# Kernel tuning notes

Hardware: AMD Instinct MI355X
Metric: run time of the kernel (lower is better)

The kernel has to match this reference:

```python
import jax, jax.numpy as jnp
import numpy as np

B, MAX_LEN, H, D = 4, 4096, 32, 128
Q_LEN = 1


def quantize_i8(x):
    # Symmetric per-(b,s,h) int8 quantization along the head dim (Array8Bit-style).
    scale = jnp.max(jnp.abs(x), axis=-1, keepdims=True) / 127.0
    scale = jnp.maximum(scale, 1e-8)
    q = jnp.clip(jnp.round(x / scale), -128, 127).astype(jnp.int8)
    return q, scale


def setup_inputs() -> dict:
    key = jax.random.key(0)
    k0, k1, k2, k3 = jax.random.split(key, 4)
    return {
        "cached_key": jax.random.normal(k0, (B, MAX_LEN, H, D), dtype=jnp.float32),
        "cached_value": jax.random.normal(k1, (B, MAX_LEN, H, D), dtype=jnp.float32),
        "key": jax.random.normal(k2, (B, Q_LEN, H, D), dtype=jnp.float32),
        "value": jax.random.normal(k3, (B, Q_LEN, H, D), dtype=jnp.float32),
        "attention_mask": jnp.ones((B, 1, Q_LEN, MAX_LEN), dtype=jnp.bool_),
        "cache_index": 2048,
    }


def reference(cached_key, cached_value, key, value, attention_mask, cache_index):
    # --- FlaxAttentionModule._concatenate_to_cache (non-sharded decode path) ---
    max_length = cached_key.shape[1]
    cur_index = jnp.asarray(cache_index, dtype=jnp.int32)
    num_updated = key.shape[1]  # query_states.shape[1]

    # KV-cache write: dynamic_update_slice at (0, cur_index, 0, 0)
    key_out = jax.lax.dynamic_update_slice(cached_key, key, (0, cur_index, 0, 0))
    value_out = jax.lax.dynamic_update_slice(cached_value, value, (0, cur_index, 0, 0))

    # pad_mask: positions < cur_index + num_updated are valid
    pad_mask = jnp.broadcast_to(
        jnp.arange(max_length) < cur_index + num_updated,
        (cached_key.shape[0], 1, num_updated, max_length),
    )
    # combine_masks == logical AND of boolean masks
    attn_mask_out = jnp.logical_and(pad_mask, attention_mask)

    # Inline int8 quantization of the updated cache (quantize_kv_cache path)
    key_q, key_scale = quantize_i8(key_out)
    value_q, value_scale = quantize_i8(value_out)

    return key_out, value_out, attn_mask_out, key_q, key_scale, value_q, value_scale
```

## Files before the change

kernel.cpp:

```cpp
#include <hip/hip_runtime.h>

constexpr long long N_ELEM  = 4LL * 4096 * 32 * 128;
constexpr long long N_ROWS  = 4LL * 4096 * 32;
constexpr long long MASK_N  = 4LL * 4096;
constexpr long long SCALE_N = N_ROWS;


typedef float vf4 __attribute__((ext_vector_type(4)));

__global__ __launch_bounds__(256) void kv_update_quant_kernel(
    const float* __restrict__ cached_key,
    const float* __restrict__ cached_value,
    const float* __restrict__ key_new,
    const float* __restrict__ value_new,
    const int*   __restrict__ cache_index,
    float* __restrict__ out)
{
    const int cur  = cache_index[0];
    const int hw   = threadIdx.x >> 5;
    const int lane = threadIdx.x & 31;

    const long long row0 = (((long long)blockIdx.x * 8 + hw) << 2);
    const bool isv = row0 >= N_ROWS;
    const long long r0 = isv ? row0 - N_ROWS : row0;

    const int h0 = (int)(r0 & 31);
    const int s  = (int)((r0 >> 5) & 4095);
    const long long b = r0 >> 17;

    const float* src;
    if (s == cur) {
        src = (isv ? value_new : key_new) + (((b << 5) + (long long)h0) << 7);
    } else {
        src = (isv ? cached_value : cached_key) + (r0 << 7);
    }
    src += (lane << 2);

    vf4 v[4];
#pragma unroll
    for (int j = 0; j < 4; ++j)
        v[j] = __builtin_nontemporal_load(reinterpret_cast<const vf4*>(src + (j << 7)));

    float sc[4];
#pragma unroll
    for (int j = 0; j < 4; ++j) {
        float m = fmaxf(fmaxf(fabsf(v[j].x), fabsf(v[j].y)),
                        fmaxf(fabsf(v[j].z), fabsf(v[j].w)));
#pragma unroll
        for (int off = 16; off >= 1; off >>= 1)
            m = fmaxf(m, __shfl_xor(m, off));
        sc[j] = fmaxf(m / 127.0f, 1e-8f);
    }

    float* out_p = out + (isv ? N_ELEM : 0) + (r0 << 7) + (lane << 2);
    float* q_p   = out + 2 * N_ELEM + MASK_N + (isv ? (N_ELEM + SCALE_N) : 0)
                   + (r0 << 7) + (lane << 2);

#pragma unroll
    for (int j = 0; j < 4; ++j) {
        __builtin_nontemporal_store(v[j], reinterpret_cast<vf4*>(out_p + (j << 7)));
        vf4 q;
        q.x = fminf(fmaxf(rintf(v[j].x / sc[j]), -128.0f), 127.0f);
        q.y = fminf(fmaxf(rintf(v[j].y / sc[j]), -128.0f), 127.0f);
        q.z = fminf(fmaxf(rintf(v[j].z / sc[j]), -128.0f), 127.0f);
        q.w = fminf(fmaxf(rintf(v[j].w / sc[j]), -128.0f), 127.0f);
        __builtin_nontemporal_store(q, reinterpret_cast<vf4*>(q_p + (j << 7)));
    }

    if (lane == 0) {
        float* s_p = out + 3 * N_ELEM + MASK_N + (isv ? (N_ELEM + SCALE_N) : 0) + r0;
        vf4 sv;
        sv.x = sc[0]; sv.y = sc[1]; sv.z = sc[2]; sv.w = sc[3];
        __builtin_nontemporal_store(sv, reinterpret_cast<vf4*>(s_p));
    }
}

__global__ __launch_bounds__(256) void mask_kernel(
    const int* __restrict__ attention_mask,
    const int* __restrict__ cache_index,
    float* __restrict__ out_mask)
{
    const int i = blockIdx.x * 256 + threadIdx.x;
    if (i < (int)MASK_N) {
        const int pos = i & 4095;
        const bool pad = pos < (cache_index[0] + 1);
        const bool am  = attention_mask[i] != 0;
        out_mask[i] = (pad && am) ? 1.0f : 0.0f;
    }
}

extern "C" void kernel_launch(void* const* d_in, const int* in_sizes, int n_in,
                              void* d_out, int out_size, void* d_ws, size_t ws_size,
                              hipStream_t stream) {
    const float* cached_key   = (const float*)d_in[0];
    const float* cached_value = (const float*)d_in[1];
    const float* key_new      = (const float*)d_in[2];
    const float* value_new    = (const float*)d_in[3];
    const int*   attn_mask    = (const int*)d_in[4];
    const int*   cache_index  = (const int*)d_in[5];
    float* out = (float*)d_out;

    kv_update_quant_kernel<<<32768, 256, 0, stream>>>(
        cached_key, cached_value, key_new, value_new, cache_index, out);

    mask_kernel<<<(int)(MASK_N / 256), 256, 0, stream>>>(
        attn_mask, cache_index, out + 2 * N_ELEM);
}
```

Before: 1.332 ms.

## Use persistent-style workers looping over 16 row-quads with register prefetch

Each half-wave now handles 16 consecutive row-quads in a loop instead of one, and the grid shrinks from 32768 to 2048 blocks. Inside the loop the next quad's loads are issued before the current quad's reduction, quantization and stores, a software double-buffer in registers. The aim is to cut block launch overhead and overlap memory latency. The cost is fewer resident waves to hide latency and more register pressure from holding two quads.

```diff
diff --git a/kernel.cpp b/kernel.cpp
--- a/kernel.cpp
+++ b/kernel.cpp
@@ -7,6 +7,9 @@
 
 
 typedef float vf4 __attribute__((ext_vector_type(4)));
+
+constexpr int QUADS_PER_WORKER = 16;
+constexpr int NUM_BLOCKS = 2048;
 
 __global__ __launch_bounds__(256) void kv_update_quant_kernel(
     const float* __restrict__ cached_key,
@@ -20,58 +23,81 @@
     const int hw   = threadIdx.x >> 5;
     const int lane = threadIdx.x & 31;
 
-    const long long row0 = (((long long)blockIdx.x * 8 + hw) << 2);
-    const bool isv = row0 >= N_ROWS;
-    const long long r0 = isv ? row0 - N_ROWS : row0;
+    const long long w  = (long long)blockIdx.x * 8 + hw;
+    const long long q0 = w * QUADS_PER_WORKER;
 
-    const int h0 = (int)(r0 & 31);
-    const int s  = (int)((r0 >> 5) & 4095);
-    const long long b = r0 >> 17;
+    const bool isv = (q0 << 2) >= N_ROWS;
+    const long long rbase = (q0 << 2) - (isv ? N_ROWS : 0);
 
-    const float* src;
-    if (s == cur) {
-        src = (isv ? value_new : key_new) + (((b << 5) + (long long)h0) << 7);
-    } else {
-        src = (isv ? cached_value : cached_key) + (r0 << 7);
-    }
-    src += (lane << 2);
+    const float* cached = isv ? cached_value : cached_key;
+    const float* knew   = isv ? value_new   : key_new;
+
+    float* out_base = out + (isv ? N_ELEM : 0);
+    float* q_base   = out + 2 * N_ELEM + MASK_N + (isv ? (N_ELEM + SCALE_N) : 0);
+    float* s_base   = out + 3 * N_ELEM + MASK_N + (isv ? (N_ELEM + SCALE_N) : 0);
+
+    auto src_for = [&](long long r0) -> const float* {
+        const int s = (int)((r0 >> 5) & 4095);
+        if (s == cur) {
+            const long long b = r0 >> 17;
+            const int h0 = (int)(r0 & 31);
+            return knew + (((b << 5) + (long long)h0) << 7) + (lane << 2);
+        }
+        return cached + (r0 << 7) + (lane << 2);
+    };
 
     vf4 v[4];
-#pragma unroll
-    for (int j = 0; j < 4; ++j)
-        v[j] = __builtin_nontemporal_load(reinterpret_cast<const vf4*>(src + (j << 7)));
-
-    float sc[4];
-#pragma unroll
-    for (int j = 0; j < 4; ++j) {
-        float m = fmaxf(fmaxf(fabsf(v[j].x), fabsf(v[j].y)),
-                        fmaxf(fabsf(v[j].z), fabsf(v[j].w)));
-#pragma unroll
-        for (int off = 16; off >= 1; off >>= 1)
-            m = fmaxf(m, __shfl_xor(m, off));
-        sc[j] = fmaxf(m / 127.0f, 1e-8f);
+    {
+        const float* src = src_for(rbase);
+        #pragma unroll
+        for (int j = 0; j < 4; ++j)
+            v[j] = __builtin_nontemporal_load(reinterpret_cast<const vf4*>(src + (j << 7)));
     }
 
-    float* out_p = out + (isv ? N_ELEM : 0) + (r0 << 7) + (lane << 2);
-    float* q_p   = out + 2 * N_ELEM + MASK_N + (isv ? (N_ELEM + SCALE_N) : 0)
-                   + (r0 << 7) + (lane << 2);
+    for (int i = 0; i < QUADS_PER_WORKER; ++i) {
+        const long long r0 = rbase + ((long long)i << 2);
 
-#pragma unroll
-    for (int j = 0; j < 4; ++j) {
-        __builtin_nontemporal_store(v[j], reinterpret_cast<vf4*>(out_p + (j << 7)));
-        vf4 q;
-        q.x = fminf(fmaxf(rintf(v[j].x / sc[j]), -128.0f), 127.0f);
-        q.y = fminf(fmaxf(rintf(v[j].y / sc[j]), -128.0f), 127.0f);
-        q.z = fminf(fmaxf(rintf(v[j].z / sc[j]), -128.0f), 127.0f);
-        q.w = fminf(fmaxf(rintf(v[j].w / sc[j]), -128.0f), 127.0f);
-        __builtin_nontemporal_store(q, reinterpret_cast<vf4*>(q_p + (j << 7)));
-    }
+        vf4 nv[4];
+        if (i + 1 < QUADS_PER_WORKER) {
+            const float* nsrc = src_for(r0 + 4);
+            #pragma unroll
+            for (int j = 0; j < 4; ++j)
+                nv[j] = __builtin_nontemporal_load(reinterpret_cast<const vf4*>(nsrc + (j << 7)));
+        }
 
-    if (lane == 0) {
-        float* s_p = out + 3 * N_ELEM + MASK_N + (isv ? (N_ELEM + SCALE_N) : 0) + r0;
-        vf4 sv;
-        sv.x = sc[0]; sv.y = sc[1]; sv.z = sc[2]; sv.w = sc[3];
-        __builtin_nontemporal_store(sv, reinterpret_cast<vf4*>(s_p));
+        float sc[4];
+        #pragma unroll
+        for (int j = 0; j < 4; ++j) {
+            float m = fmaxf(fmaxf(fabsf(v[j].x), fabsf(v[j].y)),
+                            fmaxf(fabsf(v[j].z), fabsf(v[j].w)));
+            #pragma unroll
+            for (int off = 16; off >= 1; off >>= 1)
+                m = fmaxf(m, __shfl_xor(m, off));
+            sc[j] = fmaxf(m / 127.0f, 1e-8f);
+        }
+
+        float* out_p = out_base + (r0 << 7) + (lane << 2);
+        float* q_p   = q_base   + (r0 << 7) + (lane << 2);
+
+        #pragma unroll
+        for (int j = 0; j < 4; ++j) {
+            __builtin_nontemporal_store(v[j], reinterpret_cast<vf4*>(out_p + (j << 7)));
+            vf4 q;
+            q.x = fminf(fmaxf(rintf(v[j].x / sc[j]), -128.0f), 127.0f);
+            q.y = fminf(fmaxf(rintf(v[j].y / sc[j]), -128.0f), 127.0f);
+            q.z = fminf(fmaxf(rintf(v[j].z / sc[j]), -128.0f), 127.0f);
+            q.w = fminf(fmaxf(rintf(v[j].w / sc[j]), -128.0f), 127.0f);
+            __builtin_nontemporal_store(q, reinterpret_cast<vf4*>(q_p + (j << 7)));
+        }
+
+        if (lane == 0) {
+            vf4 sv;
+            sv.x = sc[0]; sv.y = sc[1]; sv.z = sc[2]; sv.w = sc[3];
+            __builtin_nontemporal_store(sv, reinterpret_cast<vf4*>(s_base + r0));
+        }
+
+        #pragma unroll
+        for (int j = 0; j < 4; ++j) v[j] = nv[j];
     }
 }
 
@@ -100,7 +126,7 @@
     const int*   cache_index  = (const int*)d_in[5];
     float* out = (float*)d_out;
 
-    kv_update_quant_kernel<<<32768, 256, 0, stream>>>(
+    kv_update_quant_kernel<<<NUM_BLOCKS, 256, 0, stream>>>(
         cached_key, cached_value, key_new, value_new, cache_index, out);
 
     mask_kernel<<<(int)(MASK_N / 256), 256, 0, stream>>>(
```

New measurement: 1.355 ms. Within noise of the previous version (+1.7%).
